# Kernel tuning notes

Hardware: AMD Instinct MI355X
Metric: run time of the kernel (lower is better)

## Reference

```python
import jax, jax.numpy as jnp
import numpy as np

B, L, D, H, E = 8, 256, 128, 6, 32

def setup_inputs() -> dict:
    key = jax.random.key(0)
    ks = jax.random.split(key, 9)
    s = 0.02
    return {
        "x": jax.random.normal(ks[0], (B, L, D), jnp.float32),
        "weight_adj": jax.random.uniform(ks[1], (B, H, L, L), jnp.float32),
        "e": jax.random.normal(ks[2], (B, L, L, E), jnp.float32),
        "W_w": jax.random.normal(ks[3], (D, D), jnp.float32) * s,
        "W_b": jax.random.normal(ks[4], (D,), jnp.float32) * s,
        "Wx_w": jax.random.normal(ks[5], (H, H + 2 * D + E), jnp.float32) * s,
        "Wx_b": jax.random.normal(ks[6], (H,), jnp.float32) * s,
        "Wxx_w": jax.random.normal(ks[7], (D, D), jnp.float32) * s,
        "Wxx_b": jax.random.normal(ks[8], (D,), jnp.float32) * s,
    }

def reference(x, weight_adj, e, W_w, W_b, Wx_w, Wx_b, Wxx_w, Wxx_b):
    d = x.shape[-1]
    h = weight_adj.shape[1]
    # mean over heads, then graph conv + linear + relu
    adj_avg = weight_adj.mean(axis=1)                      # [B,L,L]
    gcn = jax.nn.relu(jnp.einsum('bij,bjd->bid', adj_avg, x) @ W_w.T + W_b)  # [B,L,d]
    # Wx applied to cat([weight_adj_perm, node_i, node_j, e], -1), decomposed
    # column-wise so the huge [B,L,L,2d+H+E] concat is never materialized;
    # math is identical to Linear(cat(...)).
    Wa  = Wx_w[:, :h]                 # [H,H]
    Wn1 = Wx_w[:, h:h + d]            # [H,d]
    Wn2 = Wx_w[:, h + d:h + 2 * d]    # [H,d]
    We  = Wx_w[:, h + 2 * d:]         # [H,E]
    adj_term = jnp.einsum('bhij,kh->bijk', weight_adj, Wa)   # [B,L,L,H]
    n1 = gcn @ Wn1.T                                          # [B,L,H] (row node)
    n2 = gcn @ Wn2.T                                          # [B,L,H] (col node)
    e_term = jnp.einsum('bije,ke->bijk', e, We)               # [B,L,L,H]
    new_adj = adj_term + n1[:, :, None, :] + n2[:, None, :, :] + e_term + Wx_b
    new_adj = jnp.transpose(new_adj, (0, 3, 1, 2))            # [B,H,L,L]
    out = gcn @ Wxx_w.T + Wxx_b                               # [B,L,d]
    return out, new_adj
```

## Files before the change

### kernel.cpp

```cpp
#include <hip/hip_runtime.h>

#define Bn 8
#define Ln 256
#define Dn 128
#define Hn 6
#define En 32
#define WXROW (Hn + 2*Dn + En)
#define ROWS 4

__global__ __launch_bounds__(256) void k_gcn(
    const float* __restrict__ x, const float* __restrict__ wadj,
    const float* __restrict__ W_w, const float* __restrict__ W_b,
    const float* __restrict__ Wx_w,
    const float* __restrict__ Wxx_w, const float* __restrict__ Wxx_b,
    float* __restrict__ out, float* __restrict__ n1_ws, float* __restrict__ n2_ws)
{
    __shared__ float adj[ROWS][Ln];
    __shared__ float part[8][ROWS][Dn];
    __shared__ float t_s[ROWS][Dn];
    __shared__ float g_s[ROWS][Dn];

    const int t  = threadIdx.x;
    const int b  = blockIdx.x >> 6;
    const int i0 = (blockIdx.x & 63) * ROWS;

    const int q  = t >> 5;
    const int d4 = t & 31;
    const float4* xp4 = (const float4*)(x + (size_t)b * Ln * Dn) + d4;
    const int j0 = q * 32;

    float4 xpre[8];
    #pragma unroll
    for (int p = 0; p < 8; ++p)
        xpre[p] = xp4[(size_t)(j0 + p) * 32];

    {
        const int r  = t >> 6;
        const int j4 = t & 63;
        const float4* w4 = (const float4*)wadj;
        float4 s = {0.f, 0.f, 0.f, 0.f};
        #pragma unroll
        for (int h = 0; h < Hn; ++h) {
            const float4 v = w4[(((size_t)b * Hn + h) * Ln + (i0 + r)) * 64 + j4];
            s.x += v.x; s.y += v.y; s.z += v.z; s.w += v.w;
        }
        const float inv_h = 1.0f / 6.0f;
        s.x *= inv_h; s.y *= inv_h; s.z *= inv_h; s.w *= inv_h;
        ((float4*)&adj[0][0])[r * 64 + j4] = s;
    }
    __syncthreads();

    {
        float4 acc[ROWS];
        #pragma unroll
        for (int r = 0; r < ROWS; ++r) acc[r] = {0.f, 0.f, 0.f, 0.f};
        const float4* adj4 = (const float4*)&adj[0][0];

        #pragma unroll
        for (int blk4 = 0; blk4 < 8; ++blk4) {
            const int j = j0 + blk4 * 4;
            float4 xv0, xv1, xv2, xv3;
            if (blk4 < 2) {
                xv0 = xpre[blk4 * 4 + 0]; xv1 = xpre[blk4 * 4 + 1];
                xv2 = xpre[blk4 * 4 + 2]; xv3 = xpre[blk4 * 4 + 3];
            } else {
                xv0 = xp4[(size_t)(j + 0) * 32];
                xv1 = xp4[(size_t)(j + 1) * 32];
                xv2 = xp4[(size_t)(j + 2) * 32];
                xv3 = xp4[(size_t)(j + 3) * 32];
            }
            #pragma unroll
            for (int r = 0; r < ROWS; ++r) {
                const float4 a = adj4[r * 64 + (j >> 2)];
                float4 v = acc[r];
                v.x = fmaf(a.x, xv0.x, v.x); v.y = fmaf(a.x, xv0.y, v.y);
                v.z = fmaf(a.x, xv0.z, v.z); v.w = fmaf(a.x, xv0.w, v.w);
                v.x = fmaf(a.y, xv1.x, v.x); v.y = fmaf(a.y, xv1.y, v.y);
                v.z = fmaf(a.y, xv1.z, v.z); v.w = fmaf(a.y, xv1.w, v.w);
                v.x = fmaf(a.z, xv2.x, v.x); v.y = fmaf(a.z, xv2.y, v.y);
                v.z = fmaf(a.z, xv2.z, v.z); v.w = fmaf(a.z, xv2.w, v.w);
                v.x = fmaf(a.w, xv3.x, v.x); v.y = fmaf(a.w, xv3.y, v.y);
                v.z = fmaf(a.w, xv3.z, v.z); v.w = fmaf(a.w, xv3.w, v.w);
                acc[r] = v;
            }
        }
        #pragma unroll
        for (int r = 0; r < ROWS; ++r)
            ((float4*)&part[q][r][0])[d4] = acc[r];
    }
    __syncthreads();

    const int dd = t & 127;
    const int ss = t >> 7;

    float4 wpre[8];
    {
        const float4* wr = (const float4*)(W_w + (size_t)dd * Dn);
        #pragma unroll
        for (int p = 0; p < 8; ++p) wpre[p] = wr[p];
    }

    {
        #pragma unroll
        for (int rq = 0; rq < 2; ++rq) {
            const int r = ss + rq * 2;
            float s = 0.f;
            #pragma unroll
            for (int qq = 0; qq < 8; ++qq) s += part[qq][r][dd];
            t_s[r][dd] = s;
        }
    }
    __syncthreads();

    {
        const int r0 = ss, r1 = ss + 2;
        float a0 = W_b[dd], a1 = a0;
        const float4* wr = (const float4*)(W_w + (size_t)dd * Dn);
        const float4* t0 = (const float4*)&t_s[r0][0];
        const float4* t1 = (const float4*)&t_s[r1][0];
        #pragma unroll
        for (int c4 = 0; c4 < Dn / 4; ++c4) {
            const float4 w = (c4 < 8) ? wpre[c4] : wr[c4];
            const float4 u0 = t0[c4];
            const float4 u1 = t1[c4];
            a0 = fmaf(u0.x, w.x, a0); a0 = fmaf(u0.y, w.y, a0);
            a0 = fmaf(u0.z, w.z, a0); a0 = fmaf(u0.w, w.w, a0);
            a1 = fmaf(u1.x, w.x, a1); a1 = fmaf(u1.y, w.y, a1);
            a1 = fmaf(u1.z, w.z, a1); a1 = fmaf(u1.w, w.w, a1);
        }
        g_s[r0][dd] = fmaxf(a0, 0.f);
        g_s[r1][dd] = fmaxf(a1, 0.f);
    }
    {
        const float4* wr = (const float4*)(Wxx_w + (size_t)dd * Dn);
        #pragma unroll
        for (int p = 0; p < 8; ++p) wpre[p] = wr[p];
    }
    __syncthreads();

    {
        const int r0 = ss, r1 = ss + 2;
        float a0 = Wxx_b[dd], a1 = a0;
        const float4* wr = (const float4*)(Wxx_w + (size_t)dd * Dn);
        const float4* g0 = (const float4*)&g_s[r0][0];
        const float4* g1 = (const float4*)&g_s[r1][0];
        #pragma unroll
        for (int c4 = 0; c4 < Dn / 4; ++c4) {
            const float4 w = (c4 < 8) ? wpre[c4] : wr[c4];
            const float4 u0 = g0[c4];
            const float4 u1 = g1[c4];
            a0 = fmaf(u0.x, w.x, a0); a0 = fmaf(u0.y, w.y, a0);
            a0 = fmaf(u0.z, w.z, a0); a0 = fmaf(u0.w, w.w, a0);
            a1 = fmaf(u1.x, w.x, a1); a1 = fmaf(u1.y, w.y, a1);
            a1 = fmaf(u1.z, w.z, a1); a1 = fmaf(u1.w, w.w, a1);
        }
        out[((size_t)b * Ln + (i0 + r0)) * Dn + dd] = a0;
        out[((size_t)b * Ln + (i0 + r1)) * Dn + dd] = a1;
    }

    if (t < ROWS * 2 * Hn) {
        const int r  = t / (2 * Hn);
        const int kk = t % (2 * Hn);
        const int k  = (kk < Hn) ? kk : (kk - Hn);
        const bool isn2 = (kk >= Hn);
        const float* wrow = Wx_w + (size_t)k * WXROW + Hn + (isn2 ? Dn : 0);
        float acc = 0.f;
        #pragma unroll 8
        for (int c = 0; c < Dn; ++c)
            acc = fmaf(g_s[r][c], wrow[c], acc);
        const size_t idx = ((size_t)b * Hn + k) * Ln + (i0 + r);
        if (isn2) n2_ws[idx] = acc;
        else      n1_ws[idx] = acc;
    }
}

#define EPAD 33
__global__ __launch_bounds__(256) void k_adj(
    const float* __restrict__ wadj, const float* __restrict__ e,
    const float* __restrict__ Wx_w, const float* __restrict__ Wx_b,
    const float* __restrict__ n1_ws, const float* __restrict__ n2_ws,
    float* __restrict__ new_adj)
{
    __shared__ float e_lds[128 * EPAD];
    __shared__ float Wa_s[Hn][Hn];
    __shared__ float We_s[Hn][En];
    __shared__ float bias_n1[Hn];

    const int t = threadIdx.x;
    const int b = blockIdx.x >> 8;
    const int i = blockIdx.x & 255;

    const float4* ep4 = (const float4*)(e + (((size_t)b * Ln + i) * Ln) * En);

    float4 A[4], Bv[4];
    #pragma unroll
    for (int p = 0; p < 4; ++p) A[p]  = ep4[t + p * 256];
    #pragma unroll
    for (int p = 0; p < 4; ++p) Bv[p] = ep4[1024 + t + p * 256];

    if (t < Hn * Hn) {
        const int k = t / Hn, h = t % Hn;
        Wa_s[k][h] = Wx_w[(size_t)k * WXROW + h];
    }
    if (t >= 64 && t < 64 + Hn * En) {
        const int q = t - 64, k = q / En, c = q % En;
        We_s[k][c] = Wx_w[(size_t)k * WXROW + Hn + 2 * Dn + c];
    }
    if (t >= 32 && t < 32 + Hn) {
        const int k = t - 32;
        bias_n1[k] = Wx_b[k] + n1_ws[((size_t)b * Hn + k) * Ln + i];
    }

    #pragma unroll
    for (int p = 0; p < 4; ++p) {
        const int idx = t + p * 256;
        const int j = idx >> 3;
        const int c = (idx & 7) * 4;
        float* dst = &e_lds[j * EPAD + c];
        dst[0] = A[p].x; dst[1] = A[p].y; dst[2] = A[p].z; dst[3] = A[p].w;
    }
    __syncthreads();

    const int s  = t >> 7;
    const int jl = t & 127;

    #pragma unroll
    for (int cH = 0; cH < 2; ++cH) {
        const int j = cH * 128 + jl;

        float wv[Hn];
        #pragma unroll
        for (int h = 0; h < Hn; ++h)
            wv[h] = wadj[(((size_t)b * Hn + h) * Ln + i) * Ln + j];

        float n2v[3];
        #pragma unroll
        for (int kq = 0; kq < 3; ++kq)
            n2v[kq] = n2_ws[((size_t)b * Hn + s * 3 + kq) * Ln + j];

        const float* ev = &e_lds[jl * EPAD];
        float evr[En];
        #pragma unroll
        for (int c = 0; c < En; ++c) evr[c] = ev[c];

        #pragma unroll
        for (int kq = 0; kq < 3; ++kq) {
            const int k = s * 3 + kq;
            float acc = bias_n1[k] + n2v[kq];
            #pragma unroll
            for (int h = 0; h < Hn; ++h)
                acc = fmaf(wv[h], Wa_s[k][h], acc);
            #pragma unroll
            for (int c = 0; c < En; ++c)
                acc = fmaf(evr[c], We_s[k][c], acc);
            new_adj[(((size_t)b * Hn + k) * Ln + i) * Ln + j] = acc;
        }

        if (cH == 0) {
            __syncthreads();
            #pragma unroll
            for (int p = 0; p < 4; ++p) {
                const int idx = t + p * 256;
                const int jj = idx >> 3;
                const int c = (idx & 7) * 4;
                float* dst = &e_lds[jj * EPAD + c];
                dst[0] = Bv[p].x; dst[1] = Bv[p].y;
                dst[2] = Bv[p].z; dst[3] = Bv[p].w;
            }
            __syncthreads();
        }
    }
}

extern "C" void kernel_launch(void* const* d_in, const int* in_sizes, int n_in,
                              void* d_out, int out_size, void* d_ws, size_t ws_size,
                              hipStream_t stream) {
    const float* x      = (const float*)d_in[0];
    const float* wadj   = (const float*)d_in[1];
    const float* e      = (const float*)d_in[2];
    const float* W_w    = (const float*)d_in[3];
    const float* W_b    = (const float*)d_in[4];
    const float* Wx_w   = (const float*)d_in[5];
    const float* Wx_b   = (const float*)d_in[6];
    const float* Wxx_w  = (const float*)d_in[7];
    const float* Wxx_b  = (const float*)d_in[8];

    float* out      = (float*)d_out;
    float* new_adj  = out + (size_t)Bn * Ln * Dn;

    float* n1_ws = (float*)d_ws;
    float* n2_ws = n1_ws + (size_t)Bn * Hn * Ln;

    k_gcn<<<Bn * (Ln / ROWS), 256, 0, stream>>>(x, wadj, W_w, W_b, Wx_w,
                                                Wxx_w, Wxx_b, out, n1_ws, n2_ws);
    k_adj<<<Bn * Ln, 256, 0, stream>>>(wadj, e, Wx_w, Wx_b, n1_ws, n2_ws, new_adj);
}
```

Baseline: 147.4 us.

## Fuse GCN and adjacency kernels into one cooperative kernel with grid sync

```diff
diff --git a/kernel.cpp b/kernel.cpp
--- a/kernel.cpp
+++ b/kernel.cpp
@@ -1,4 +1,7 @@
 #include <hip/hip_runtime.h>
+#include <hip/hip_cooperative_groups.h>
+
+namespace cg = cooperative_groups;
 
 #define Bn 8
 #define Ln 256
@@ -8,71 +11,327 @@
 #define WXROW (Hn + 2*Dn + En)
 #define ROWS 4
 
-__global__ __launch_bounds__(256) void k_gcn(
+struct P1 {
+    float adj[ROWS][Ln];
+    float part[8][ROWS][Dn];
+    float t_s[ROWS][Dn];
+    float g_s[ROWS][Dn];
+};
+struct P2 {
+    float e_lds[128 * 33];
+    float Wa[Hn][Hn];
+    float We[Hn][En];
+    float bias[Hn];
+};
+union SharedU { P1 p1; P2 p2; };
+
+__device__ __forceinline__ void load_wx(const float* __restrict__ Wx_w,
+                                        const float* __restrict__ Wx_b,
+                                        P2& sp, int t)
+{
+    if (t < Hn * Hn)
+        sp.Wa[t / Hn][t % Hn] = Wx_w[(size_t)(t / Hn) * WXROW + (t % Hn)];
+    if (t >= 64 && t < 64 + Hn * En) {
+        const int q = t - 64;
+        sp.We[q / En][q % En] = Wx_w[(size_t)(q / En) * WXROW + Hn + 2 * Dn + (q % En)];
+    }
+    if (t >= 32 && t < 32 + Hn)
+        sp.bias[t - 32] = Wx_b[t - 32];
+}
+
+__device__ __forceinline__ void unit_acc(
+    const float* __restrict__ wadj, const float4 A[4], const float4 Bv[4],
+    P2& sp, int b, int i, int t, float acc[2][3])
+{
+    const int s = t >> 7, jl = t & 127;
+    __syncthreads();
+    #pragma unroll
+    for (int p = 0; p < 4; ++p) {
+        const int idx = t + p * 256;
+        const int j = idx >> 3, c = (idx & 7) * 4;
+        float* dst = &sp.e_lds[j * 33 + c];
+        dst[0] = A[p].x; dst[1] = A[p].y; dst[2] = A[p].z; dst[3] = A[p].w;
+    }
+    __syncthreads();
+    #pragma unroll
+    for (int h = 0; h < 2; ++h) {
+        const int j = h * 128 + jl;
+        float wv[Hn];
+        #pragma unroll
+        for (int hh = 0; hh < Hn; ++hh)
+            wv[hh] = wadj[(((size_t)b * Hn + hh) * Ln + i) * Ln + j];
+        const float* ev = &sp.e_lds[jl * 33];
+        #pragma unroll
+        for (int kq = 0; kq < 3; ++kq) {
+            const int k = s * 3 + kq;
+            float a = sp.bias[k];
+            #pragma unroll
+            for (int hh = 0; hh < Hn; ++hh)
+                a = fmaf(wv[hh], sp.Wa[k][hh], a);
+            #pragma unroll
+            for (int c = 0; c < En; ++c)
+                a = fmaf(ev[c], sp.We[k][c], a);
+            acc[h][kq] = a;
+        }
+        if (h == 0) {
+            __syncthreads();
+            #pragma unroll
+            for (int p = 0; p < 4; ++p) {
+                const int idx = t + p * 256;
+                const int j2 = idx >> 3, c = (idx & 7) * 4;
+                float* dst = &sp.e_lds[j2 * 33 + c];
+                dst[0] = Bv[p].x; dst[1] = Bv[p].y; dst[2] = Bv[p].z; dst[3] = Bv[p].w;
+            }
+            __syncthreads();
+        }
+    }
+}
+
+__device__ __forceinline__ void unit_store(
+    const float* __restrict__ n1_ws, const float* __restrict__ n2_ws,
+    float* __restrict__ new_adj, int b, int i, int t, const float acc[2][3])
+{
+    const int s = t >> 7, jl = t & 127;
+    #pragma unroll
+    for (int kq = 0; kq < 3; ++kq) {
+        const int k = s * 3 + kq;
+        const float n1v = n1_ws[((size_t)b * Hn + k) * Ln + i];
+        #pragma unroll
+        for (int h = 0; h < 2; ++h) {
+            const int j = h * 128 + jl;
+            const float v = acc[h][kq] + n1v + n2_ws[((size_t)b * Hn + k) * Ln + j];
+            new_adj[(((size_t)b * Hn + k) * Ln + i) * Ln + j] = v;
+        }
+    }
+}
+
+__global__ __launch_bounds__(256, 4) void k_fused(
+    const float* __restrict__ x, const float* __restrict__ wadj,
+    const float* __restrict__ e,
+    const float* __restrict__ W_w, const float* __restrict__ W_b,
+    const float* __restrict__ Wx_w, const float* __restrict__ Wx_b,
+    const float* __restrict__ Wxx_w, const float* __restrict__ Wxx_b,
+    float* __restrict__ out, float* __restrict__ new_adj,
+    float* __restrict__ n1_ws, float* __restrict__ n2_ws)
+{
+    __shared__ SharedU sh;
+    const int t = threadIdx.x;
+    const int blk = blockIdx.x;
+
+    float acc[2][2][3];
+
+    if (blk >= 512) {
+        load_wx(Wx_w, Wx_b, sh.p2, t);
+        #pragma unroll
+        for (int u = 0; u < 2; ++u) {
+            const int idx = blk * 2 + u;
+            const int b = idx >> 8, i = idx & 255;
+            const float4* ep4 = (const float4*)(e + (((size_t)b * Ln + i) * Ln) * En);
+            float4 A[4], Bv[4];
+            #pragma unroll
+            for (int p = 0; p < 4; ++p) A[p]  = ep4[t + p * 256];
+            #pragma unroll
+            for (int p = 0; p < 4; ++p) Bv[p] = ep4[1024 + t + p * 256];
+            unit_acc(wadj, A, Bv, sh.p2, b, i, t, acc[u]);
+        }
+    } else {
+        const int b  = blk >> 6;
+        const int i0 = (blk & 63) * ROWS;
+
+        {
+            const int r = t >> 6, j4 = t & 63;
+            const float4* w4 = (const float4*)wadj;
+            float4 s4 = {0.f, 0.f, 0.f, 0.f};
+            #pragma unroll
+            for (int h = 0; h < Hn; ++h) {
+                const float4 v = w4[(((size_t)b * Hn + h) * Ln + (i0 + r)) * 64 + j4];
+                s4.x += v.x; s4.y += v.y; s4.z += v.z; s4.w += v.w;
+            }
+            const float inv_h = 1.0f / 6.0f;
+            s4.x *= inv_h; s4.y *= inv_h; s4.z *= inv_h; s4.w *= inv_h;
+            ((float4*)&sh.p1.adj[0][0])[r * 64 + j4] = s4;
+        }
+        __syncthreads();
+
+        {
+            const int q = t >> 5, d4 = t & 31;
+            float4 a4[ROWS];
+            #pragma unroll
+            for (int r = 0; r < ROWS; ++r) a4[r] = {0.f, 0.f, 0.f, 0.f};
+            const float4* xp4  = (const float4*)(x + (size_t)b * Ln * Dn) + d4;
+            const float4* adj4 = (const float4*)&sh.p1.adj[0][0];
+            const int j0 = q * 32;
+            #pragma unroll
+            for (int jj4 = 0; jj4 < 8; ++jj4) {
+                const int j = j0 + jj4 * 4;
+                const float4 xv0 = xp4[(size_t)(j + 0) * 32];
+                const float4 xv1 = xp4[(size_t)(j + 1) * 32];
+                const float4 xv2 = xp4[(size_t)(j + 2) * 32];
+                const float4 xv3 = xp4[(size_t)(j + 3) * 32];
+                #pragma unroll
+                for (int r = 0; r < ROWS; ++r) {
+                    const float4 a = adj4[r * 64 + (j >> 2)];
+                    float4 v = a4[r];
+                    v.x = fmaf(a.x, xv0.x, v.x); v.y = fmaf(a.x, xv0.y, v.y);
+                    v.z = fmaf(a.x, xv0.z, v.z); v.w = fmaf(a.x, xv0.w, v.w);
+                    v.x = fmaf(a.y, xv1.x, v.x); v.y = fmaf(a.y, xv1.y, v.y);
+                    v.z = fmaf(a.y, xv1.z, v.z); v.w = fmaf(a.y, xv1.w, v.w);
+                    v.x = fmaf(a.z, xv2.x, v.x); v.y = fmaf(a.z, xv2.y, v.y);
+                    v.z = fmaf(a.z, xv2.z, v.z); v.w = fmaf(a.z, xv2.w, v.w);
+                    v.x = fmaf(a.w, xv3.x, v.x); v.y = fmaf(a.w, xv3.y, v.y);
+                    v.z = fmaf(a.w, xv3.z, v.z); v.w = fmaf(a.w, xv3.w, v.w);
+                    a4[r] = v;
+                }
+            }
+            #pragma unroll
+            for (int r = 0; r < ROWS; ++r)
+                ((float4*)&sh.p1.part[q][r][0])[d4] = a4[r];
+        }
+        __syncthreads();
+
+        {
+            const int dd = t & 127, rr = t >> 7;
+            #pragma unroll
+            for (int rq = 0; rq < 2; ++rq) {
+                const int r = rr + rq * 2;
+                float s = 0.f;
+                #pragma unroll
+                for (int qq = 0; qq < 8; ++qq) s += sh.p1.part[qq][r][dd];
+                sh.p1.t_s[r][dd] = s;
+            }
+        }
+        __syncthreads();
+
+        {
+            const int ss = t >> 7, dd = t & 127;
+            const int r0 = ss, r1 = ss + 2;
+            float a0 = W_b[dd], a1 = a0;
+            const float4* wr = (const float4*)(W_w + (size_t)dd * Dn);
+            const float4* t0 = (const float4*)&sh.p1.t_s[r0][0];
+            const float4* t1 = (const float4*)&sh.p1.t_s[r1][0];
+            #pragma unroll 8
+            for (int c4 = 0; c4 < Dn / 4; ++c4) {
+                const float4 w = wr[c4];
+                const float4 u0 = t0[c4];
+                const float4 u1 = t1[c4];
+                a0 = fmaf(u0.x, w.x, a0); a0 = fmaf(u0.y, w.y, a0);
+                a0 = fmaf(u0.z, w.z, a0); a0 = fmaf(u0.w, w.w, a0);
+                a1 = fmaf(u1.x, w.x, a1); a1 = fmaf(u1.y, w.y, a1);
+                a1 = fmaf(u1.z, w.z, a1); a1 = fmaf(u1.w, w.w, a1);
+            }
+            sh.p1.g_s[r0][dd] = fmaxf(a0, 0.f);
+            sh.p1.g_s[r1][dd] = fmaxf(a1, 0.f);
+        }
+        __syncthreads();
+
+        {
+            const int ss = t >> 7, dd = t & 127;
+            const int r0 = ss, r1 = ss + 2;
+            float a0 = Wxx_b[dd], a1 = a0;
+            const float4* wr = (const float4*)(Wxx_w + (size_t)dd * Dn);
+            const float4* g0 = (const float4*)&sh.p1.g_s[r0][0];
+            const float4* g1 = (const float4*)&sh.p1.g_s[r1][0];
+            #pragma unroll 8
+            for (int c4 = 0; c4 < Dn / 4; ++c4) {
+                const float4 w = wr[c4];
+                const float4 u0 = g0[c4];
+                const float4 u1 = g1[c4];
+                a0 = fmaf(u0.x, w.x, a0); a0 = fmaf(u0.y, w.y, a0);
+                a0 = fmaf(u0.z, w.z, a0); a0 = fmaf(u0.w, w.w, a0);
+                a1 = fmaf(u1.x, w.x, a1); a1 = fmaf(u1.y, w.y, a1);
+                a1 = fmaf(u1.z, w.z, a1); a1 = fmaf(u1.w, w.w, a1);
+            }
+            out[((size_t)b * Ln + (i0 + r0)) * Dn + dd] = a0;
+            out[((size_t)b * Ln + (i0 + r1)) * Dn + dd] = a1;
+        }
+
+        if (t < ROWS * 2 * Hn) {
+            const int r  = t / (2 * Hn);
+            const int kk = t % (2 * Hn);
+            const int k  = (kk < Hn) ? kk : (kk - Hn);
+            const bool isn2 = (kk >= Hn);
+            const float* wrow = Wx_w + (size_t)k * WXROW + Hn + (isn2 ? Dn : 0);
+            float a = 0.f;
+            #pragma unroll 8
+            for (int c = 0; c < Dn; ++c)
+                a = fmaf(sh.p1.g_s[r][c], wrow[c], a);
+            const size_t widx = ((size_t)b * Hn + k) * Ln + (i0 + r);
+            if (isn2) n2_ws[widx] = a;
+            else      n1_ws[widx] = a;
+        }
+        __threadfence();
+    }
+
+    cg::this_grid().sync();
+
+    if (blk >= 512) {
+        #pragma unroll
+        for (int u = 0; u < 2; ++u) {
+            const int idx = blk * 2 + u;
+            unit_store(n1_ws, n2_ws, new_adj, idx >> 8, idx & 255, t, acc[u]);
+        }
+    } else {
+        load_wx(Wx_w, Wx_b, sh.p2, t);
+        #pragma unroll
+        for (int u = 0; u < 2; ++u) {
+            const int idx = blk * 2 + u;
+            const int b = idx >> 8, i = idx & 255;
+            const float4* ep4 = (const float4*)(e + (((size_t)b * Ln + i) * Ln) * En);
+            float4 A[4], Bv[4];
+            #pragma unroll
+            for (int p = 0; p < 4; ++p) A[p]  = ep4[t + p * 256];
+            #pragma unroll
+            for (int p = 0; p < 4; ++p) Bv[p] = ep4[1024 + t + p * 256];
+            unit_acc(wadj, A, Bv, sh.p2, b, i, t, acc[u]);
+            unit_store(n1_ws, n2_ws, new_adj, b, i, t, acc[u]);
+        }
+    }
+}
+
+__global__ __launch_bounds__(256) void k_gcn_fb(
     const float* __restrict__ x, const float* __restrict__ wadj,
     const float* __restrict__ W_w, const float* __restrict__ W_b,
     const float* __restrict__ Wx_w,
     const float* __restrict__ Wxx_w, const float* __restrict__ Wxx_b,
     float* __restrict__ out, float* __restrict__ n1_ws, float* __restrict__ n2_ws)
 {
-    __shared__ float adj[ROWS][Ln];
-    __shared__ float part[8][ROWS][Dn];
-    __shared__ float t_s[ROWS][Dn];
-    __shared__ float g_s[ROWS][Dn];
-
+    __shared__ P1 sp;
     const int t  = threadIdx.x;
     const int b  = blockIdx.x >> 6;
     const int i0 = (blockIdx.x & 63) * ROWS;
-
-    const int q  = t >> 5;
-    const int d4 = t & 31;
-    const float4* xp4 = (const float4*)(x + (size_t)b * Ln * Dn) + d4;
-    const int j0 = q * 32;
-
-    float4 xpre[8];
-    #pragma unroll
-    for (int p = 0; p < 8; ++p)
-        xpre[p] = xp4[(size_t)(j0 + p) * 32];
-
     {
-        const int r  = t >> 6;
-        const int j4 = t & 63;
+        const int r = t >> 6, j4 = t & 63;
         const float4* w4 = (const float4*)wadj;
-        float4 s = {0.f, 0.f, 0.f, 0.f};
+        float4 s4 = {0.f, 0.f, 0.f, 0.f};
         #pragma unroll
         for (int h = 0; h < Hn; ++h) {
             const float4 v = w4[(((size_t)b * Hn + h) * Ln + (i0 + r)) * 64 + j4];
-            s.x += v.x; s.y += v.y; s.z += v.z; s.w += v.w;
+            s4.x += v.x; s4.y += v.y; s4.z += v.z; s4.w += v.w;
         }
         const float inv_h = 1.0f / 6.0f;
-        s.x *= inv_h; s.y *= inv_h; s.z *= inv_h; s.w *= inv_h;
-        ((float4*)&adj[0][0])[r * 64 + j4] = s;
-    }
-    __syncthreads();
-
+        s4.x *= inv_h; s4.y *= inv_h; s4.z *= inv_h; s4.w *= inv_h;
+        ((float4*)&sp.adj[0][0])[r * 64 + j4] = s4;
+    }
+    __syncthreads();
     {
-        float4 acc[ROWS];
-        #pragma unroll
-        for (int r = 0; r < ROWS; ++r) acc[r] = {0.f, 0.f, 0.f, 0.f};
-        const float4* adj4 = (const float4*)&adj[0][0];
-
-        #pragma unroll
-        for (int blk4 = 0; blk4 < 8; ++blk4) {
-            const int j = j0 + blk4 * 4;
-            float4 xv0, xv1, xv2, xv3;
-            if (blk4 < 2) {
-                xv0 = xpre[blk4 * 4 + 0]; xv1 = xpre[blk4 * 4 + 1];
-                xv2 = xpre[blk4 * 4 + 2]; xv3 = xpre[blk4 * 4 + 3];
-            } else {
-                xv0 = xp4[(size_t)(j + 0) * 32];
-                xv1 = xp4[(size_t)(j + 1) * 32];
-                xv2 = xp4[(size_t)(j + 2) * 32];
-                xv3 = xp4[(size_t)(j + 3) * 32];
-            }
+        const int q = t >> 5, d4 = t & 31;
+        float4 a4[ROWS];
+        #pragma unroll
+        for (int r = 0; r < ROWS; ++r) a4[r] = {0.f, 0.f, 0.f, 0.f};
+        const float4* xp4  = (const float4*)(x + (size_t)b * Ln * Dn) + d4;
+        const float4* adj4 = (const float4*)&sp.adj[0][0];
+        const int j0 = q * 32;
+        #pragma unroll
+        for (int jj4 = 0; jj4 < 8; ++jj4) {
+            const int j = j0 + jj4 * 4;
+            const float4 xv0 = xp4[(size_t)(j + 0) * 32];
+            const float4 xv1 = xp4[(size_t)(j + 1) * 32];
+            const float4 xv2 = xp4[(size_t)(j + 2) * 32];
+            const float4 xv3 = xp4[(size_t)(j + 3) * 32];
             #pragma unroll
             for (int r = 0; r < ROWS; ++r) {
                 const float4 a = adj4[r * 64 + (j >> 2)];
-                float4 v = acc[r];
+                float4 v = a4[r];
                 v.x = fmaf(a.x, xv0.x, v.x); v.y = fmaf(a.x, xv0.y, v.y);
                 v.z = fmaf(a.x, xv0.z, v.z); v.w = fmaf(a.x, xv0.w, v.w);
                 v.x = fmaf(a.y, xv1.x, v.x); v.y = fmaf(a.y, xv1.y, v.y);
@@ -81,46 +340,36 @@
                 v.z = fmaf(a.z, xv2.z, v.z); v.w = fmaf(a.z, xv2.w, v.w);
                 v.x = fmaf(a.w, xv3.x, v.x); v.y = fmaf(a.w, xv3.y, v.y);
                 v.z = fmaf(a.w, xv3.z, v.z); v.w = fmaf(a.w, xv3.w, v.w);
-                acc[r] = v;
+                a4[r] = v;
             }
         }
         #pragma unroll
         for (int r = 0; r < ROWS; ++r)
-            ((float4*)&part[q][r][0])[d4] = acc[r];
-    }
-    __syncthreads();
-
-    const int dd = t & 127;
-    const int ss = t >> 7;
-
-    float4 wpre[8];
+            ((float4*)&sp.part[q][r][0])[d4] = a4[r];
+    }
+    __syncthreads();
     {
-        const float4* wr = (const float4*)(W_w + (size_t)dd * Dn);
-        #pragma unroll
-        for (int p = 0; p < 8; ++p) wpre[p] = wr[p];
-    }
-
+        const int dd = t & 127, rr = t >> 7;
+        #pragma unroll
+        for (int rq = 0; rq < 2; ++rq) {
+            const int r = rr + rq * 2;
+            float s = 0.f;
+            #pragma unroll
+            for (int qq = 0; qq < 8; ++qq) s += sp.part[qq][r][dd];
+            sp.t_s[r][dd] = s;
+        }
+    }
+    __syncthreads();
     {
-        #pragma unroll
-        for (int rq = 0; rq < 2; ++rq) {
-            const int r = ss + rq * 2;
-            float s = 0.f;
-            #pragma unroll
-            for (int qq = 0; qq < 8; ++qq) s += part[qq][r][dd];
-            t_s[r][dd] = s;
-        }
-    }
-    __syncthreads();
-
-    {
+        const int ss = t >> 7, dd = t & 127;
         const int r0 = ss, r1 = ss + 2;
         float a0 = W_b[dd], a1 = a0;
         const float4* wr = (const float4*)(W_w + (size_t)dd * Dn);
-        const float4* t0 = (const float4*)&t_s[r0][0];
-        const float4* t1 = (const float4*)&t_s[r1][0];
-        #pragma unroll
+        const float4* t0 = (const float4*)&sp.t_s[r0][0];
+        const float4* t1 = (const float4*)&sp.t_s[r1][0];
+        #pragma unroll 8
         for (int c4 = 0; c4 < Dn / 4; ++c4) {
-            const float4 w = (c4 < 8) ? wpre[c4] : wr[c4];
+            const float4 w = wr[c4];
             const float4 u0 = t0[c4];
             const float4 u1 = t1[c4];
             a0 = fmaf(u0.x, w.x, a0); a0 = fmaf(u0.y, w.y, a0);
@@ -128,25 +377,20 @@
             a1 = fmaf(u1.x, w.x, a1); a1 = fmaf(u1.y, w.y, a1);
             a1 = fmaf(u1.z, w.z, a1); a1 = fmaf(u1.w, w.w, a1);
         }
-        g_s[r0][dd] = fmaxf(a0, 0.f);
-        g_s[r1][dd] = fmaxf(a1, 0.f);
-    }
+        sp.g_s[r0][dd] = fmaxf(a0, 0.f);
+        sp.g_s[r1][dd] = fmaxf(a1, 0.f);
+    }
+    __syncthreads();
     {
-        const float4* wr = (const float4*)(Wxx_w + (size_t)dd * Dn);
-        #pragma unroll
-        for (int p = 0; p < 8; ++p) wpre[p] = wr[p];
-    }
-    __syncthreads();
-
-    {
+        const int ss = t >> 7, dd = t & 127;
         const int r0 = ss, r1 = ss + 2;
         float a0 = Wxx_b[dd], a1 = a0;
         const float4* wr = (const float4*)(Wxx_w + (size_t)dd * Dn);
-        const float4* g0 = (const float4*)&g_s[r0][0];
-        const float4* g1 = (const float4*)&g_s[r1][0];
-        #pragma unroll
+        const float4* g0 = (const float4*)&sp.g_s[r0][0];
+        const float4* g1 = (const float4*)&sp.g_s[r1][0];
+        #pragma unroll 8
         for (int c4 = 0; c4 < Dn / 4; ++c4) {
-            const float4 w = (c4 < 8) ? wpre[c4] : wr[c4];
+            const float4 w = wr[c4];
             const float4 u0 = g0[c4];
             const float4 u1 = g1[c4];
             a0 = fmaf(u0.x, w.x, a0); a0 = fmaf(u0.y, w.y, a0);
@@ -157,119 +401,42 @@
         out[((size_t)b * Ln + (i0 + r0)) * Dn + dd] = a0;
         out[((size_t)b * Ln + (i0 + r1)) * Dn + dd] = a1;
     }
-
     if (t < ROWS * 2 * Hn) {
         const int r  = t / (2 * Hn);
         const int kk = t % (2 * Hn);
         const int k  = (kk < Hn) ? kk : (kk - Hn);
         const bool isn2 = (kk >= Hn);
         const float* wrow = Wx_w + (size_t)k * WXROW + Hn + (isn2 ? Dn : 0);
-        float acc = 0.f;
+        float a = 0.f;
         #pragma unroll 8
         for (int c = 0; c < Dn; ++c)
-            acc = fmaf(g_s[r][c], wrow[c], acc);
-        const size_t idx = ((size_t)b * Hn + k) * Ln + (i0 + r);
-        if (isn2) n2_ws[idx] = acc;
-        else      n1_ws[idx] = acc;
-    }
-}
-
-#define EPAD 33
-__global__ __launch_bounds__(256) void k_adj(
+            a = fmaf(sp.g_s[r][c], wrow[c], a);
+        const size_t widx = ((size_t)b * Hn + k) * Ln + (i0 + r);
+        if (isn2) n2_ws[widx] = a;
+        else      n1_ws[widx] = a;
+    }
+}
+
+__global__ __launch_bounds__(256) void k_adj_fb(
     const float* __restrict__ wadj, const float* __restrict__ e,
     const float* __restrict__ Wx_w, const float* __restrict__ Wx_b,
     const float* __restrict__ n1_ws, const float* __restrict__ n2_ws,
     float* __restrict__ new_adj)
 {
-    __shared__ float e_lds[128 * EPAD];
-    __shared__ float Wa_s[Hn][Hn];
-    __shared__ float We_s[Hn][En];
-    __shared__ float bias_n1[Hn];
-
+    __shared__ P2 sp;
     const int t = threadIdx.x;
     const int b = blockIdx.x >> 8;
     const int i = blockIdx.x & 255;
-
+    load_wx(Wx_w, Wx_b, sp, t);
     const float4* ep4 = (const float4*)(e + (((size_t)b * Ln + i) * Ln) * En);
-
     float4 A[4], Bv[4];
     #pragma unroll
     for (int p = 0; p < 4; ++p) A[p]  = ep4[t + p * 256];
     #pragma unroll
     for (int p = 0; p < 4; ++p) Bv[p] = ep4[1024 + t + p * 256];
-
-    if (t < Hn * Hn) {
-        const int k = t / Hn, h = t % Hn;
-        Wa_s[k][h] = Wx_w[(size_t)k * WXROW + h];
-    }
-    if (t >= 64 && t < 64 + Hn * En) {
-        const int q = t - 64, k = q / En, c = q % En;
-        We_s[k][c] = Wx_w[(size_t)k * WXROW + Hn + 2 * Dn + c];
-    }
-    if (t >= 32 && t < 32 + Hn) {
-        const int k = t - 32;
-        bias_n1[k] = Wx_b[k] + n1_ws[((size_t)b * Hn + k) * Ln + i];
-    }
-
-    #pragma unroll
-    for (int p = 0; p < 4; ++p) {
-        const int idx = t + p * 256;
-        const int j = idx >> 3;
-        const int c = (idx & 7) * 4;
-        float* dst = &e_lds[j * EPAD + c];
-        dst[0] = A[p].x; dst[1] = A[p].y; dst[2] = A[p].z; dst[3] = A[p].w;
-    }
-    __syncthreads();
-
-    const int s  = t >> 7;
-    const int jl = t & 127;
-
-    #pragma unroll
-    for (int cH = 0; cH < 2; ++cH) {
-        const int j = cH * 128 + jl;
-
-        float wv[Hn];
-        #pragma unroll
-        for (int h = 0; h < Hn; ++h)
-            wv[h] = wadj[(((size_t)b * Hn + h) * Ln + i) * Ln + j];
-
-        float n2v[3];
-        #pragma unroll
-        for (int kq = 0; kq < 3; ++kq)
-            n2v[kq] = n2_ws[((size_t)b * Hn + s * 3 + kq) * Ln + j];
-
-        const float* ev = &e_lds[jl * EPAD];
-        float evr[En];
-        #pragma unroll
-        for (int c = 0; c < En; ++c) evr[c] = ev[c];
-
-        #pragma unroll
-        for (int kq = 0; kq < 3; ++kq) {
-            const int k = s * 3 + kq;
-            float acc = bias_n1[k] + n2v[kq];
-            #pragma unroll
-            for (int h = 0; h < Hn; ++h)
-                acc = fmaf(wv[h], Wa_s[k][h], acc);
-            #pragma unroll
-            for (int c = 0; c < En; ++c)
-                acc = fmaf(evr[c], We_s[k][c], acc);
-            new_adj[(((size_t)b * Hn + k) * Ln + i) * Ln + j] = acc;
-        }
-
-        if (cH == 0) {
-            __syncthreads();
-            #pragma unroll
-            for (int p = 0; p < 4; ++p) {
-                const int idx = t + p * 256;
-                const int jj = idx >> 3;
-                const int c = (idx & 7) * 4;
-                float* dst = &e_lds[jj * EPAD + c];
-                dst[0] = Bv[p].x; dst[1] = Bv[p].y;
-                dst[2] = Bv[p].z; dst[3] = Bv[p].w;
-            }
-            __syncthreads();
-        }
-    }
+    float acc[2][3];
+    unit_acc(wadj, A, Bv, sp, b, i, t, acc);
+    unit_store(n1_ws, n2_ws, new_adj, b, i, t, acc);
 }
 
 extern "C" void kernel_launch(void* const* d_in, const int* in_sizes, int n_in,
@@ -291,7 +458,17 @@
     float* n1_ws = (float*)d_ws;
     float* n2_ws = n1_ws + (size_t)Bn * Hn * Ln;
 
-    k_gcn<<<Bn * (Ln / ROWS), 256, 0, stream>>>(x, wadj, W_w, W_b, Wx_w,
-                                                Wxx_w, Wxx_b, out, n1_ws, n2_ws);
-    k_adj<<<Bn * Ln, 256, 0, stream>>>(wadj, e, Wx_w, Wx_b, n1_ws, n2_ws, new_adj);
-}
+    void* args[] = {
+        (void*)&x, (void*)&wadj, (void*)&e, (void*)&W_w, (void*)&W_b,
+        (void*)&Wx_w, (void*)&Wx_b, (void*)&Wxx_w, (void*)&Wxx_b,
+        (void*)&out, (void*)&new_adj, (void*)&n1_ws, (void*)&n2_ws
+    };
+    const hipError_t err = hipLaunchCooperativeKernel(
+        reinterpret_cast<void*>(k_fused), dim3(1024), dim3(256), args, 0, stream);
+    if (err != hipSuccess) {
+        k_gcn_fb<<<Bn * (Ln / ROWS), 256, 0, stream>>>(
+            x, wadj, W_w, W_b, Wx_w, Wxx_w, Wxx_b, out, n1_ws, n2_ws);
+        k_adj_fb<<<Bn * Ln, 256, 0, stream>>>(
+            wadj, e, Wx_w, Wx_b, n1_ws, n2_ws, new_adj);
+    }
+}
```

After: 441.0 us. 199% more time.
